# Performance work log

Measured on AMD Instinct MI355X. Metric: run time of the kernel, lower is better.

## Reference

```python
import jax, jax.numpy as jnp
import numpy as np

N_HEAD = 16
N_KV_HEAD = 4
HEAD_DIM = 128
ROPE_BASE = 10000.0


def _rope_cos_sin(T, offset, dtype):
    # inv_freq: [head_dim//2]
    inv_freq = 1.0 / (ROPE_BASE ** (jnp.arange(0, HEAD_DIM, 2, dtype=jnp.float32) / HEAD_DIM))
    pos = jnp.arange(offset, offset + T, dtype=jnp.float32)
    ang = pos[:, None] * inv_freq[None, :]              # [T, hd/2]
    emb = jnp.concatenate([ang, ang], axis=-1)           # [T, hd]
    return jnp.cos(emb).astype(dtype), jnp.sin(emb).astype(dtype)


def _rotate_half(t):
    half = t.shape[-1] // 2
    return jnp.concatenate([-t[..., half:], t[..., :half]], axis=-1)


def _apply_rope(t, cos, sin):
    # t: [B, h, T, hd]; cos/sin: [T, hd]
    return t * cos[None, None] + _rotate_half(t) * sin[None, None]


def setup_inputs() -> dict:
    key = jax.random.key(0)
    ks = jax.random.split(key, 5)
    B, T, C = 4, 2048, 2048
    scale = 0.02
    return {
        "x": jax.random.normal(ks[0], (B, T, C), dtype=jnp.float32),
        "Wq": jax.random.normal(ks[1], (C, C), dtype=jnp.float32) * scale,
        "Wk": jax.random.normal(ks[2], (N_KV_HEAD * HEAD_DIM, C), dtype=jnp.float32) * scale,
        "Wv": jax.random.normal(ks[3], (N_KV_HEAD * HEAD_DIM, C), dtype=jnp.float32) * scale,
        "Wo": jax.random.normal(ks[4], (C, C), dtype=jnp.float32) * scale,
        "offset": 0,
    }


def reference(x, Wq, Wk, Wv, Wo, offset):
    B, T, C = x.shape
    n_rep = N_HEAD // N_KV_HEAD
    # projections (torch Linear: x @ W.T)
    q = (x @ Wq.T).reshape(B, T, N_HEAD, HEAD_DIM).transpose(0, 2, 1, 3)     # [B,H,T,d]
    k = (x @ Wk.T).reshape(B, T, N_KV_HEAD, HEAD_DIM).transpose(0, 2, 1, 3)  # [B,G,T,d]
    v = (x @ Wv.T).reshape(B, T, N_KV_HEAD, HEAD_DIM).transpose(0, 2, 1, 3)  # [B,G,T,d]
    cos, sin = _rope_cos_sin(T, offset, x.dtype)
    q = _apply_rope(q, cos, sin)
    k = _apply_rope(k, cos, sin)
    # GQA without materializing replicated K/V: group q heads by kv head
    qg = q.reshape(B, N_KV_HEAD, n_rep, T, HEAD_DIM)
    scale = 1.0 / jnp.sqrt(jnp.asarray(HEAD_DIM, dtype=x.dtype))
    scores = jnp.einsum('bgrtd,bgsd->bgrts', qg, k) * scale                  # [B,G,r,T,S]
    causal = jnp.tril(jnp.ones((T, T), dtype=bool))
    scores = jnp.where(causal[None, None, None], scores, jnp.asarray(-jnp.inf, dtype=scores.dtype))
    attn = jax.nn.softmax(scores, axis=-1)
    yg = jnp.einsum('bgrts,bgsd->bgrtd', attn, v)                            # [B,G,r,T,d]
    y = yg.reshape(B, N_HEAD, T, HEAD_DIM).transpose(0, 2, 1, 3).reshape(B, T, C)
    return y @ Wo.T
```

## Files before the change

### kernel.cpp

```cpp
#include <hip/hip_runtime.h>
#include <math.h>

#define BATCH 4
#define SEQ   2048
#define CDIM  2048
#define NH    16
#define NG    4
#define HD    128
#define MTOT  (BATCH*SEQ)
#define KVD   (NG*HD)

typedef __attribute__((ext_vector_type(8))) short     bf16x8;
typedef __attribute__((ext_vector_type(8))) unsigned short u16x8;
typedef __attribute__((ext_vector_type(4))) float     f32x4;
typedef unsigned short ushort_t;

static __device__ __forceinline__ unsigned short f2bf(float f) {
  unsigned u = __float_as_uint(f);
  u += 0x7FFF + ((u >> 16) & 1);
  return (unsigned short)(u >> 16);
}
static __device__ __forceinline__ float bf2f(unsigned short h) {
  return __uint_as_float(((unsigned)h) << 16);
}

#define GLOAD_LDS16(gp, lp)                                                        \
  __builtin_amdgcn_global_load_lds((const __attribute__((address_space(1))) void*)(gp), \
                                   (__attribute__((address_space(3))) void*)(lp),  \
                                   16, 0, 0)

__global__ __launch_bounds__(256) void cvt_f32_bf16(
    const float* __restrict__ s, ushort_t* __restrict__ d, int n8)
{
  int i = blockIdx.x * 256 + threadIdx.x;
  if (i >= n8) return;
  const float4* p = (const float4*)(s + (size_t)i * 8);
  float4 a = p[0], b = p[1];
  u16x8 o;
  o[0] = f2bf(a.x); o[1] = f2bf(a.y); o[2] = f2bf(a.z); o[3] = f2bf(a.w);
  o[4] = f2bf(b.x); o[5] = f2bf(b.y); o[6] = f2bf(b.z); o[7] = f2bf(b.w);
  *(u16x8*)(d + (size_t)i * 8) = o;
}

template<int OUTMODE>
__global__ __launch_bounds__(256) void gemm_bt_bf16(
    const ushort_t* __restrict__ A, const ushort_t* __restrict__ B,
    void* __restrict__ C, int M, int N, int K)
{
  __shared__ ushort_t As[128 * 32];
  __shared__ ushort_t Bs[128 * 32];
  const int tid  = threadIdx.x;
  const int lane = tid & 63, w = tid >> 6;
  const int wm = (w >> 1) * 64, wn = (w & 1) * 64;
  const int bm = blockIdx.x * 128, bn = blockIdx.y * 128;

  f32x4 acc[4][4];
#pragma unroll
  for (int m = 0; m < 4; ++m)
#pragma unroll
    for (int n = 0; n < 4; ++n) acc[m][n] = (f32x4){0.f, 0.f, 0.f, 0.f};

  const int srow = tid >> 2;
  const int scol = (tid & 3) * 8;
  const ushort_t* Ap = A + (size_t)(bm + srow) * K + scol;
  const ushort_t* Bp = B + (size_t)(bn + srow) * K + scol;

  const int fr = lane & 15, fg = lane >> 4;

  for (int k0 = 0; k0 < K; k0 += 32) {
    GLOAD_LDS16(Ap + k0,                  As + tid * 8);
    GLOAD_LDS16(Ap + (size_t)64 * K + k0, As + 2048 + tid * 8);
    GLOAD_LDS16(Bp + k0,                  Bs + tid * 8);
    GLOAD_LDS16(Bp + (size_t)64 * K + k0, Bs + 2048 + tid * 8);
    __syncthreads();

    bf16x8 av[4], bv[4];
#pragma unroll
    for (int m = 0; m < 4; ++m)
      av[m] = *(const bf16x8*)(As + (wm + m * 16 + fr) * 32 + fg * 8);
#pragma unroll
    for (int n = 0; n < 4; ++n)
      bv[n] = *(const bf16x8*)(Bs + (wn + n * 16 + fr) * 32 + fg * 8);
#pragma unroll
    for (int m = 0; m < 4; ++m)
#pragma unroll
      for (int n = 0; n < 4; ++n)
        acc[m][n] = __builtin_amdgcn_mfma_f32_16x16x32_bf16(av[m], bv[n], acc[m][n], 0, 0, 0);
    __syncthreads();
  }

  if constexpr (OUTMODE == 2) {
    __shared__ ushort_t Ct[128 * 144];
#pragma unroll
    for (int m = 0; m < 4; ++m)
#pragma unroll
      for (int n = 0; n < 4; ++n)
#pragma unroll
        for (int r = 0; r < 4; ++r)
          Ct[(wn + n * 16 + fr) * 144 + wm + m * 16 + fg * 4 + r] = f2bf(acc[m][n][r]);
    __syncthreads();
    const int col_l = tid >> 1, part = tid & 1;
    ushort_t* dst = (ushort_t*)C + (size_t)(bn + col_l) * M + bm + part * 64;
#pragma unroll
    for (int j = 0; j < 8; ++j)
      *(bf16x8*)(dst + j * 8) = *(const bf16x8*)(Ct + col_l * 144 + part * 64 + j * 8);
  } else {
#pragma unroll
    for (int m = 0; m < 4; ++m)
#pragma unroll
      for (int n = 0; n < 4; ++n)
#pragma unroll
        for (int r = 0; r < 4; ++r) {
          const int row = bm + wm + m * 16 + fg * 4 + r;
          const int col = bn + wn + n * 16 + fr;
          if (OUTMODE == 1) ((float*)C)[(size_t)row * N + col] = acc[m][n][r];
          else              ((ushort_t*)C)[(size_t)row * N + col] = f2bf(acc[m][n][r]);
        }
  }
}

__global__ __launch_bounds__(256) void rope_bf16(
    ushort_t* __restrict__ qf, ushort_t* __restrict__ kf, const int* __restrict__ off)
{
  const int idx  = blockIdx.x * 256 + threadIdx.x;
  const int qtot = MTOT * NH * (HD / 2);
  const int ktot = MTOT * NG * (HD / 2);
  if (idx >= qtot + ktot) return;

  ushort_t* buf; int row, head, i, cols;
  if (idx < qtot) {
    buf = qf; cols = NH * HD;
    row = idx / (NH * (HD / 2));
    int rem = idx % (NH * (HD / 2));
    head = rem / (HD / 2); i = rem % (HD / 2);
  } else {
    int id2 = idx - qtot;
    buf = kf; cols = NG * HD;
    row = id2 / (NG * (HD / 2));
    int rem = id2 % (NG * (HD / 2));
    head = rem / (HD / 2); i = rem % (HD / 2);
  }
  const int   t   = row % SEQ;
  const float pos = (float)(t + off[0]);
  const float inv = powf(10000.0f, -(float)i * (1.0f / 64.0f));
  const float ang = pos * inv;
  const float c = cosf(ang), s = sinf(ang);

  ushort_t* p = buf + (size_t)row * cols + head * HD + i;
  const float lo = bf2f(p[0]), hi = bf2f(p[64]);
  p[0]  = f2bf(lo * c - hi * s);
  p[64] = f2bf(hi * c + lo * s);
}

#define KPAD 136
#define VPAD 72

__global__ __launch_bounds__(256, 2) void attn_mfma(
    const ushort_t* __restrict__ qf,
    const ushort_t* __restrict__ kf,
    const ushort_t* __restrict__ vT,
    ushort_t* __restrict__ yb)
{
  __shared__ ushort_t Ks[64 * KPAD];
  __shared__ ushort_t Vt[128 * VPAD];
  __shared__ ushort_t Ps[128 * VPAD];

  const int tid  = threadIdx.x;
  const int lane = tid & 63, wq = tid >> 6;
  const int bh = blockIdx.x, b = bh >> 4, h = bh & 15, g = h >> 2;
  const int qb = blockIdx.y * 128;
  const int fr = lane & 15, fg = lane >> 4;
  const int wrow0 = qb + wq * 32;

  bf16x8 qv[2][4];
#pragma unroll
  for (int rb = 0; rb < 2; ++rb) {
    const ushort_t* qp = qf + (size_t)(b * SEQ + wrow0 + rb * 16 + fr) * CDIM + h * HD + fg * 8;
#pragma unroll
    for (int ds = 0; ds < 4; ++ds) qv[rb][ds] = *(const bf16x8*)(qp + ds * 32);
  }

  f32x4 o[2][8];
#pragma unroll
  for (int rb = 0; rb < 2; ++rb)
#pragma unroll
    for (int n = 0; n < 8; ++n) o[rb][n] = (f32x4){0.f, 0.f, 0.f, 0.f};
  float mrow[2][4], lrow[2][4];
#pragma unroll
  for (int rb = 0; rb < 2; ++rb)
#pragma unroll
    for (int r = 0; r < 4; ++r) { mrow[rb][r] = -1e30f; lrow[rb][r] = 0.f; }

  const float K2 = 0.12751743671f;
  const int nkv = qb / 64 + 2;

  const ushort_t* vtb0 = vT + (size_t)(g * HD) * MTOT + (size_t)b * SEQ;
  const ushort_t* kfb  = kf + (size_t)(b * SEQ) * KVD + g * HD;

  bf16x8 kpre[4], vpre[4];

  auto prefetch = [&](int s0n) {
#pragma unroll
    for (int it = 0; it < 4; ++it) {
      const int f4 = tid + it * 256;
      kpre[it] = *(const bf16x8*)(kfb + (size_t)(s0n + (f4 >> 4)) * KVD + (f4 & 15) * 8);
    }
#pragma unroll
    for (int it = 0; it < 4; ++it) {
      const int f4 = tid + it * 256;
      vpre[it] = *(const bf16x8*)(vtb0 + s0n + (size_t)(f4 >> 3) * MTOT + (f4 & 7) * 8);
    }
  };
  auto writetile = [&]() {
#pragma unroll
    for (int it = 0; it < 4; ++it) {
      const int f4 = tid + it * 256;
      *(bf16x8*)(Ks + (f4 >> 4) * KPAD + (f4 & 15) * 8) = kpre[it];
    }
#pragma unroll
    for (int it = 0; it < 4; ++it) {
      const int f4 = tid + it * 256;
      *(bf16x8*)(Vt + (f4 >> 3) * VPAD + (f4 & 7) * 8) = vpre[it];
    }
  };

  prefetch(0);
  writetile();
  __syncthreads();

  for (int kb = 0; kb < nkv; ++kb) {
    const int s0 = kb * 64;
    const bool last = (kb + 1 >= nkv);
    if (!last) prefetch(s0 + 64);

    if (s0 <= wrow0 + 31) {
      f32x4 st[2][4];
#pragma unroll
      for (int rb = 0; rb < 2; ++rb)
#pragma unroll
        for (int n = 0; n < 4; ++n) st[rb][n] = (f32x4){0.f, 0.f, 0.f, 0.f};
      __builtin_amdgcn_s_setprio(1);
#pragma unroll
      for (int ds = 0; ds < 4; ++ds)
#pragma unroll
        for (int n = 0; n < 4; ++n) {
          bf16x8 kvf = *(const bf16x8*)(Ks + (n * 16 + fr) * KPAD + ds * 32 + fg * 8);
          st[0][n] = __builtin_amdgcn_mfma_f32_16x16x32_bf16(qv[0][ds], kvf, st[0][n], 0, 0, 0);
          st[1][n] = __builtin_amdgcn_mfma_f32_16x16x32_bf16(qv[1][ds], kvf, st[1][n], 0, 0, 0);
        }
      __builtin_amdgcn_s_setprio(0);

      const bool nomask = (s0 + 63 <= wrow0);
      float es[2][4];
#pragma unroll
      for (int rb = 0; rb < 2; ++rb)
#pragma unroll
        for (int r = 0; r < 4; ++r) {
          const int grow = wrow0 + rb * 16 + fg * 4 + r;
          float sv[4], mx = -1e30f;
#pragma unroll
          for (int n = 0; n < 4; ++n) {
            float v = st[rb][n][r];
            if (!nomask) {
              const int col = s0 + n * 16 + fr;
              v = (col <= grow) ? v : -1e30f;
            }
            sv[n] = v; mx = fmaxf(mx, v);
          }
          mx = fmaxf(mx, __shfl_xor(mx, 1, 64));
          mx = fmaxf(mx, __shfl_xor(mx, 2, 64));
          mx = fmaxf(mx, __shfl_xor(mx, 4, 64));
          mx = fmaxf(mx, __shfl_xor(mx, 8, 64));
          const float mnew = fmaxf(mrow[rb][r], mx);
          es[rb][r] = exp2f((mrow[rb][r] - mnew) * K2);
          float sum = 0.f;
          const int prow = (wq * 32 + rb * 16 + fg * 4 + r) * VPAD;
#pragma unroll
          for (int n = 0; n < 4; ++n) {
            const float p = exp2f((sv[n] - mnew) * K2);
            sum += p;
            Ps[prow + n * 16 + fr] = f2bf(p);
          }
          sum += __shfl_xor(sum, 1, 64);
          sum += __shfl_xor(sum, 2, 64);
          sum += __shfl_xor(sum, 4, 64);
          sum += __shfl_xor(sum, 8, 64);
          lrow[rb][r] = lrow[rb][r] * es[rb][r] + sum;
          mrow[rb][r] = mnew;
        }
#pragma unroll
      for (int rb = 0; rb < 2; ++rb)
#pragma unroll
        for (int n = 0; n < 8; ++n)
#pragma unroll
          for (int r = 0; r < 4; ++r) o[rb][n][r] *= es[rb][r];

      __builtin_amdgcn_s_setprio(1);
#pragma unroll
      for (int ks = 0; ks < 2; ++ks) {
        bf16x8 pa0 = *(const bf16x8*)(Ps + (wq * 32 + fr) * VPAD + ks * 32 + fg * 8);
        bf16x8 pa1 = *(const bf16x8*)(Ps + (wq * 32 + 16 + fr) * VPAD + ks * 32 + fg * 8);
#pragma unroll
        for (int n = 0; n < 8; ++n) {
          bf16x8 vbf = *(const bf16x8*)(Vt + (n * 16 + fr) * VPAD + ks * 32 + fg * 8);
          o[0][n] = __builtin_amdgcn_mfma_f32_16x16x32_bf16(pa0, vbf, o[0][n], 0, 0, 0);
          o[1][n] = __builtin_amdgcn_mfma_f32_16x16x32_bf16(pa1, vbf, o[1][n], 0, 0, 0);
        }
      }
      __builtin_amdgcn_s_setprio(0);
    }

    __syncthreads();
    if (!last) writetile();
    __syncthreads();
  }

#pragma unroll
  for (int rb = 0; rb < 2; ++rb)
#pragma unroll
    for (int n = 0; n < 8; ++n)
#pragma unroll
      for (int r = 0; r < 4; ++r) {
        const int row = qb + wq * 32 + rb * 16 + fg * 4 + r;
        const int col = h * HD + n * 16 + fr;
        yb[(size_t)(b * SEQ + row) * CDIM + col] = f2bf(o[rb][n][r] / lrow[rb][r]);
      }
}

extern "C" void kernel_launch(void* const* d_in, const int* in_sizes, int n_in,
                              void* d_out, int out_size, void* d_ws, size_t ws_size,
                              hipStream_t stream) {
  const float* x  = (const float*)d_in[0];
  const float* Wq = (const float*)d_in[1];
  const float* Wk = (const float*)d_in[2];
  const float* Wv = (const float*)d_in[3];
  const float* Wo = (const float*)d_in[4];
  const int*   off = (const int*)d_in[5];
  float* out = (float*)d_out;

  ushort_t* xb  = (ushort_t*)d_ws;
  ushort_t* wqb = xb  + (size_t)MTOT * CDIM;
  ushort_t* wkb = wqb + (size_t)CDIM * CDIM;
  ushort_t* wvb = wkb + (size_t)KVD * CDIM;
  ushort_t* wob = wvb + (size_t)KVD * CDIM;
  ushort_t* qb_ = wob + (size_t)CDIM * CDIM;
  ushort_t* kb_ = qb_ + (size_t)MTOT * CDIM;
  ushort_t* vT_ = kb_ + (size_t)MTOT * KVD;
  ushort_t* yb_ = vT_ + (size_t)MTOT * KVD;

  dim3 blk(256);

  int n8;
  n8 = MTOT * CDIM / 8; cvt_f32_bf16<<<(n8 + 255) / 256, blk, 0, stream>>>(x,  xb,  n8);
  n8 = CDIM * CDIM / 8; cvt_f32_bf16<<<(n8 + 255) / 256, blk, 0, stream>>>(Wq, wqb, n8);
  n8 = KVD  * CDIM / 8; cvt_f32_bf16<<<(n8 + 255) / 256, blk, 0, stream>>>(Wk, wkb, n8);
  n8 = KVD  * CDIM / 8; cvt_f32_bf16<<<(n8 + 255) / 256, blk, 0, stream>>>(Wv, wvb, n8);
  n8 = CDIM * CDIM / 8; cvt_f32_bf16<<<(n8 + 255) / 256, blk, 0, stream>>>(Wo, wob, n8);

  gemm_bt_bf16<0><<<dim3(MTOT / 128, CDIM / 128), blk, 0, stream>>>(xb, wqb, qb_, MTOT, CDIM, CDIM);
  gemm_bt_bf16<0><<<dim3(MTOT / 128, KVD / 128),  blk, 0, stream>>>(xb, wkb, kb_, MTOT, KVD, CDIM);
  gemm_bt_bf16<2><<<dim3(MTOT / 128, KVD / 128),  blk, 0, stream>>>(xb, wvb, vT_, MTOT, KVD, CDIM);

  const int total_pairs = MTOT * (NH + NG) * (HD / 2);
  rope_bf16<<<(total_pairs + 255) / 256, blk, 0, stream>>>(qb_, kb_, off);

  attn_mfma<<<dim3(BATCH * NH, SEQ / 128), blk, 0, stream>>>(qb_, kb_, vT_, yb_);

  gemm_bt_bf16<1><<<dim3(MTOT / 128, CDIM / 128), blk, 0, stream>>>(yb_, wob, out, MTOT, CDIM, CDIM);
}
```

Before: 720.2 us.

## Table-driven vectorized RoPE, lazy softmax rescale, reversed causal block order in attention

RoPE is split into a small cos/sin table kernel plus a vectorized apply kernel that processes 8 pairs per thread, replacing per-element powf/sin/cos and scalar bf16 accesses. In attention, the online-softmax rescale of O and l is skipped unless some row's max grows past a threshold. Row sums are reduced across lanes only once, at the end. Query blocks are launched heaviest-first to improve load balance under the causal mask, and occupancy is raised to 3 blocks per CU with a smaller P pad. The threshold-based lazy rescale risks exp overflow or precision loss if scores jump by less than the threshold repeatedly, and the higher occupancy target may cause register spills.

```diff
diff --git a/kernel.cpp b/kernel.cpp
--- a/kernel.cpp
+++ b/kernel.cpp
@@ -119,43 +119,50 @@
   }
 }
 
-__global__ __launch_bounds__(256) void rope_bf16(
-    ushort_t* __restrict__ qf, ushort_t* __restrict__ kf, const int* __restrict__ off)
-{
-  const int idx  = blockIdx.x * 256 + threadIdx.x;
-  const int qtot = MTOT * NH * (HD / 2);
-  const int ktot = MTOT * NG * (HD / 2);
-  if (idx >= qtot + ktot) return;
-
-  ushort_t* buf; int row, head, i, cols;
-  if (idx < qtot) {
-    buf = qf; cols = NH * HD;
-    row = idx / (NH * (HD / 2));
-    int rem = idx % (NH * (HD / 2));
-    head = rem / (HD / 2); i = rem % (HD / 2);
-  } else {
-    int id2 = idx - qtot;
-    buf = kf; cols = NG * HD;
-    row = id2 / (NG * (HD / 2));
-    int rem = id2 % (NG * (HD / 2));
-    head = rem / (HD / 2); i = rem % (HD / 2);
-  }
-  const int   t   = row % SEQ;
-  const float pos = (float)(t + off[0]);
-  const float inv = powf(10000.0f, -(float)i * (1.0f / 64.0f));
-  const float ang = pos * inv;
-  const float c = cosf(ang), s = sinf(ang);
-
-  ushort_t* p = buf + (size_t)row * cols + head * HD + i;
-  const float lo = bf2f(p[0]), hi = bf2f(p[64]);
-  p[0]  = f2bf(lo * c - hi * s);
-  p[64] = f2bf(hi * c + lo * s);
+__global__ __launch_bounds__(256) void rope_table(
+    float2* __restrict__ tab, const int* __restrict__ off)
+{
+  int idx = blockIdx.x * 256 + threadIdx.x;
+  if (idx >= SEQ * 64) return;
+  int t = idx >> 6, i = idx & 63;
+  float ang = (float)(t + off[0]) * powf(10000.0f, -(float)i * (1.0f / 64.0f));
+  tab[idx] = make_float2(cosf(ang), sinf(ang));
+}
+
+__global__ __launch_bounds__(256) void rope_apply(
+    ushort_t* __restrict__ qf, ushort_t* __restrict__ kf,
+    const float2* __restrict__ tab)
+{
+  int idx = blockIdx.x * 256 + threadIdx.x;
+  if (idx >= MTOT * 20 * 8) return;
+  const int i8 = idx & 7;
+  int rem = idx >> 3;
+  const int head = rem % 20, row = rem / 20;
+
+  ushort_t* p = (head < NH)
+      ? qf + (size_t)row * CDIM + head * HD + i8 * 8
+      : kf + (size_t)row * KVD + (head - NH) * HD + i8 * 8;
+
+  const int t = row & (SEQ - 1);
+  const float2* tp = tab + t * 64 + i8 * 8;
+  u16x8 lo = *(const u16x8*)p, hi = *(const u16x8*)(p + 64);
+  u16x8 nlo, nhi;
+#pragma unroll
+  for (int j = 0; j < 8; ++j) {
+    const float2 cs = tp[j];
+    const float l = bf2f(lo[j]), h_ = bf2f(hi[j]);
+    nlo[j] = f2bf(l * cs.x - h_ * cs.y);
+    nhi[j] = f2bf(h_ * cs.x + l * cs.y);
+  }
+  *(u16x8*)p = nlo;
+  *(u16x8*)(p + 64) = nhi;
 }
 
 #define KPAD 136
 #define VPAD 72
-
-__global__ __launch_bounds__(256, 2) void attn_mfma(
+#define PPAD 66
+
+__global__ __launch_bounds__(256, 3) void attn_mfma(
     const ushort_t* __restrict__ qf,
     const ushort_t* __restrict__ kf,
     const ushort_t* __restrict__ vT,
@@ -163,12 +170,12 @@
 {
   __shared__ ushort_t Ks[64 * KPAD];
   __shared__ ushort_t Vt[128 * VPAD];
-  __shared__ ushort_t Ps[128 * VPAD];
+  __shared__ ushort_t Ps[128 * PPAD];
 
   const int tid  = threadIdx.x;
   const int lane = tid & 63, wq = tid >> 6;
   const int bh = blockIdx.x, b = bh >> 4, h = bh & 15, g = h >> 2;
-  const int qb = blockIdx.y * 128;
+  const int qb = (gridDim.y - 1 - blockIdx.y) * 128;
   const int fr = lane & 15, fg = lane >> 4;
   const int wrow0 = qb + wq * 32;
 
@@ -192,6 +199,7 @@
     for (int r = 0; r < 4; ++r) { mrow[rb][r] = -1e30f; lrow[rb][r] = 0.f; }
 
   const float K2 = 0.12751743671f;
+  const float RTHR = 62.0f;
   const int nkv = qb / 64 + 2;
 
   const ushort_t* vtb0 = vT + (size_t)(g * HD) * MTOT + (size_t)b * SEQ;
@@ -251,55 +259,67 @@
       __builtin_amdgcn_s_setprio(0);
 
       const bool nomask = (s0 + 63 <= wrow0);
-      float es[2][4];
+      float mx_a[2][4];
+      bool grew = false;
 #pragma unroll
       for (int rb = 0; rb < 2; ++rb)
 #pragma unroll
         for (int r = 0; r < 4; ++r) {
           const int grow = wrow0 + rb * 16 + fg * 4 + r;
-          float sv[4], mx = -1e30f;
+          float mx = -1e30f;
 #pragma unroll
           for (int n = 0; n < 4; ++n) {
             float v = st[rb][n][r];
             if (!nomask) {
               const int col = s0 + n * 16 + fr;
               v = (col <= grow) ? v : -1e30f;
+              st[rb][n][r] = v;
             }
-            sv[n] = v; mx = fmaxf(mx, v);
+            mx = fmaxf(mx, v);
           }
           mx = fmaxf(mx, __shfl_xor(mx, 1, 64));
           mx = fmaxf(mx, __shfl_xor(mx, 2, 64));
           mx = fmaxf(mx, __shfl_xor(mx, 4, 64));
           mx = fmaxf(mx, __shfl_xor(mx, 8, 64));
-          const float mnew = fmaxf(mrow[rb][r], mx);
-          es[rb][r] = exp2f((mrow[rb][r] - mnew) * K2);
+          mx_a[rb][r] = mx;
+          grew = grew || (mx > mrow[rb][r] + RTHR);
+        }
+
+      if (__any(grew)) {
+#pragma unroll
+        for (int rb = 0; rb < 2; ++rb)
+#pragma unroll
+          for (int r = 0; r < 4; ++r) {
+            const float mnew = fmaxf(mrow[rb][r], mx_a[rb][r]);
+            const float es = exp2f((mrow[rb][r] - mnew) * K2);
+            lrow[rb][r] *= es;
+            mrow[rb][r] = mnew;
+#pragma unroll
+            for (int n = 0; n < 8; ++n) o[rb][n][r] *= es;
+          }
+      }
+
+#pragma unroll
+      for (int rb = 0; rb < 2; ++rb)
+#pragma unroll
+        for (int r = 0; r < 4; ++r) {
+          const float m = mrow[rb][r];
           float sum = 0.f;
-          const int prow = (wq * 32 + rb * 16 + fg * 4 + r) * VPAD;
+          const int prow = (wq * 32 + rb * 16 + fg * 4 + r) * PPAD;
 #pragma unroll
           for (int n = 0; n < 4; ++n) {
-            const float p = exp2f((sv[n] - mnew) * K2);
+            const float p = exp2f((st[rb][n][r] - m) * K2);
             sum += p;
             Ps[prow + n * 16 + fr] = f2bf(p);
           }
-          sum += __shfl_xor(sum, 1, 64);
-          sum += __shfl_xor(sum, 2, 64);
-          sum += __shfl_xor(sum, 4, 64);
-          sum += __shfl_xor(sum, 8, 64);
-          lrow[rb][r] = lrow[rb][r] * es[rb][r] + sum;
-          mrow[rb][r] = mnew;
-        }
-#pragma unroll
-      for (int rb = 0; rb < 2; ++rb)
-#pragma unroll
-        for (int n = 0; n < 8; ++n)
-#pragma unroll
-          for (int r = 0; r < 4; ++r) o[rb][n][r] *= es[rb][r];
+          lrow[rb][r] += sum;
+        }
 
       __builtin_amdgcn_s_setprio(1);
 #pragma unroll
       for (int ks = 0; ks < 2; ++ks) {
-        bf16x8 pa0 = *(const bf16x8*)(Ps + (wq * 32 + fr) * VPAD + ks * 32 + fg * 8);
-        bf16x8 pa1 = *(const bf16x8*)(Ps + (wq * 32 + 16 + fr) * VPAD + ks * 32 + fg * 8);
+        bf16x8 pa0 = *(const bf16x8*)(Ps + (wq * 32 + fr) * PPAD + ks * 32 + fg * 8);
+        bf16x8 pa1 = *(const bf16x8*)(Ps + (wq * 32 + 16 + fr) * PPAD + ks * 32 + fg * 8);
 #pragma unroll
         for (int n = 0; n < 8; ++n) {
           bf16x8 vbf = *(const bf16x8*)(Vt + (n * 16 + fr) * VPAD + ks * 32 + fg * 8);
@@ -318,13 +338,18 @@
 #pragma unroll
   for (int rb = 0; rb < 2; ++rb)
 #pragma unroll
-    for (int n = 0; n < 8; ++n)
-#pragma unroll
-      for (int r = 0; r < 4; ++r) {
-        const int row = qb + wq * 32 + rb * 16 + fg * 4 + r;
-        const int col = h * HD + n * 16 + fr;
-        yb[(size_t)(b * SEQ + row) * CDIM + col] = f2bf(o[rb][n][r] / lrow[rb][r]);
-      }
+    for (int r = 0; r < 4; ++r) {
+      float l = lrow[rb][r];
+      l += __shfl_xor(l, 1, 64);
+      l += __shfl_xor(l, 2, 64);
+      l += __shfl_xor(l, 4, 64);
+      l += __shfl_xor(l, 8, 64);
+      const float inv_l = 1.0f / l;
+      const int row = qb + wq * 32 + rb * 16 + fg * 4 + r;
+#pragma unroll
+      for (int n = 0; n < 8; ++n)
+        yb[(size_t)(b * SEQ + row) * CDIM + h * HD + n * 16 + fr] = f2bf(o[rb][n][r] * inv_l);
+    }
 }
 
 extern "C" void kernel_launch(void* const* d_in, const int* in_sizes, int n_in,
@@ -347,8 +372,11 @@
   ushort_t* kb_ = qb_ + (size_t)MTOT * CDIM;
   ushort_t* vT_ = kb_ + (size_t)MTOT * KVD;
   ushort_t* yb_ = vT_ + (size_t)MTOT * KVD;
+  float2*   tab = (float2*)(yb_ + (size_t)MTOT * CDIM);
 
   dim3 blk(256);
+
+  rope_table<<<(SEQ * 64 + 255) / 256, blk, 0, stream>>>(tab, off);
 
   int n8;
   n8 = MTOT * CDIM / 8; cvt_f32_bf16<<<(n8 + 255) / 256, blk, 0, stream>>>(x,  xb,  n8);
@@ -361,8 +389,7 @@
   gemm_bt_bf16<0><<<dim3(MTOT / 128, KVD / 128),  blk, 0, stream>>>(xb, wkb, kb_, MTOT, KVD, CDIM);
   gemm_bt_bf16<2><<<dim3(MTOT / 128, KVD / 128),  blk, 0, stream>>>(xb, wvb, vT_, MTOT, KVD, CDIM);
 
-  const int total_pairs = MTOT * (NH + NG) * (HD / 2);
-  rope_bf16<<<(total_pairs + 255) / 256, blk, 0, stream>>>(qb_, kb_, off);
+  rope_apply<<<(MTOT * 20 * 8 + 255) / 256, blk, 0, stream>>>(qb_, kb_, tab);
 
   attn_mfma<<<dim3(BATCH * NH, SEQ / 128), blk, 0, stream>>>(qb_, kb_, vT_, yb_);
 
```

After: 921.2 us. +27.9%, slower.
